# Kernel tuning notes

Measured on AMD Instinct MI355X. Metric: run time of the kernel, lower is better.

## Reference

```python
import jax, jax.numpy as jnp
import numpy as np

# Problem dims
N_LIG, N_PROT = 10000, 40000
N = N_LIG + N_PROT            # total nodes in batched graph
E = 400000                    # total edges (avg degree 8)
B = 512                       # number of pocket graphs in batch
F_LIG, F_PROT = 74, 1280      # ligand / protein node feature dims
H, D = 4, 64                  # GAT heads, per-head dim
HD = H * D                    # hidden size == PROJ_DIM == 256


def setup_inputs() -> dict:
    key = jax.random.key(0)
    ks = jax.random.split(key, 16)
    s = jnp.float32(0.05)  # keep activations tame
    return {
        "ligand_x":  jax.random.normal(ks[0], (N_LIG, F_LIG), jnp.float32),
        "protein_x": jax.random.normal(ks[1], (N_PROT, F_PROT), jnp.float32),
        "W_lig":  jax.random.normal(ks[2], (F_LIG, HD), jnp.float32) * s,
        "W_prot": jax.random.normal(ks[3], (F_PROT, HD), jnp.float32) * s,
        "W1":     jax.random.normal(ks[4], (HD, HD), jnp.float32) * s,
        "a1_src": jax.random.normal(ks[5], (H, D), jnp.float32) * s,
        "a1_dst": jax.random.normal(ks[6], (H, D), jnp.float32) * s,
        "W2":     jax.random.normal(ks[7], (HD, HD), jnp.float32) * s,
        "a2_src": jax.random.normal(ks[8], (H, D), jnp.float32) * s,
        "a2_dst": jax.random.normal(ks[9], (H, D), jnp.float32) * s,
        "W_out":  jax.random.normal(ks[10], (HD + 1, 1), jnp.float32) * s,
        "b_out":  jnp.zeros((1,), jnp.float32),
        "edge_src":  jax.random.randint(ks[11], (E,), 0, N, jnp.int32),
        "edge_dst":  jax.random.randint(ks[12], (E,), 0, N, jnp.int32),
        "graph_ids": jnp.sort(jax.random.randint(ks[13], (N,), 0, B, jnp.int32)),
        "scores":    jax.random.uniform(ks[14], (B, 1), jnp.float32),
    }


def _gat_layer(x, W, a_src, a_dst, src, dst):
    """Multi-head GAT layer over an edge list. x:[N,HD] -> [N,HD]."""
    n = x.shape[0]
    h = (x @ W).reshape(n, H, D)                               # [N,H,D]
    att_s = jnp.einsum('nhd,hd->nh', h, a_src)                 # [N,H]
    att_d = jnp.einsum('nhd,hd->nh', h, a_dst)
    e = jax.nn.leaky_relu(att_s[src] + att_d[dst], 0.2)        # [E,H]
    # edge softmax over incoming edges of each destination node
    m = jax.ops.segment_max(e, dst, num_segments=n)            # [N,H]
    w = jnp.exp(e - m[dst])                                    # [E,H]
    denom = jax.ops.segment_sum(w, dst, num_segments=n)        # [N,H]
    agg = jax.ops.segment_sum(h[src] * w[..., None], dst, num_segments=n)  # [N,H,D]
    out = agg / (denom[..., None] + 1e-9)
    return jax.nn.elu(out).reshape(n, HD)


def reference(ligand_x, protein_x, W_lig, W_prot, W1, a1_src, a1_dst,
              W2, a2_src, a2_dst, W_out, b_out,
              edge_src, edge_dst, graph_ids, scores):
    # per-node-type input projection into shared hidden space
    x = jnp.concatenate([ligand_x @ W_lig, protein_x @ W_prot], axis=0)  # [N,HD]
    h = _gat_layer(x, W1, a1_src, a1_dst, edge_src, edge_dst)
    h = _gat_layer(h, W2, a2_src, a2_dst, edge_src, edge_dst)
    # mean pooling per graph -> [B, PROJ_DIM]
    gsum = jax.ops.segment_sum(h, graph_ids, num_segments=B)
    cnt = jax.ops.segment_sum(jnp.ones((h.shape[0], 1), h.dtype), graph_ids, num_segments=B)
    pooled = gsum / jnp.maximum(cnt, 1.0)
    # concat docking score, final linear (dropout is identity at eval)
    feat = jnp.concatenate([pooled, scores], axis=1)           # [B, PROJ_DIM+1]
    return feat @ W_out + b_out                                 # [B,1]
```

## Files before the change

kernel.cpp:

```cpp
#include <hip/hip_runtime.h>
#include <hip/hip_bf16.h>

#define N_LIG   10000
#define N_PROT  40000
#define NN      50000
#define EDGES   400000
#define BATCH   512
#define F_LIG   74
#define F_PROT  1280
#define HD      256
#define HEADS   4
#define DIM     64

typedef __bf16 bf16x8 __attribute__((ext_vector_type(8)));
typedef __bf16 bf16x4 __attribute__((ext_vector_type(4)));
typedef float  f32x4  __attribute__((ext_vector_type(4)));


__global__ void k_hist(const int* __restrict__ dst, int* __restrict__ counts, int E) {
    int e = blockIdx.x * blockDim.x + threadIdx.x;
    if (e < E) atomicAdd(&counts[dst[e]], 1);
}

__global__ __launch_bounds__(1024) void k_scan1(const int* __restrict__ counts,
                                                int* __restrict__ incl,
                                                int* __restrict__ bsum, int N) {
    __shared__ int tmp[1024];
    int i = blockIdx.x * 1024 + threadIdx.x;
    int v = (i < N) ? counts[i] : 0;
    tmp[threadIdx.x] = v;
    __syncthreads();
    for (int off = 1; off < 1024; off <<= 1) {
        int add = (threadIdx.x >= (unsigned)off) ? tmp[threadIdx.x - off] : 0;
        __syncthreads();
        tmp[threadIdx.x] += add;
        __syncthreads();
    }
    if (i < N) incl[i] = tmp[threadIdx.x];
    if (threadIdx.x == 1023) bsum[blockIdx.x] = tmp[1023];
}

__global__ void k_scan2(int* __restrict__ bsum, int nb, int* __restrict__ row_ptr, int N, int E) {
    if (threadIdx.x == 0 && blockIdx.x == 0) {
        int run = 0;
        for (int i = 0; i < nb; ++i) { int v = bsum[i]; bsum[i] = run; run += v; }
        row_ptr[N] = E;
    }
}

__global__ __launch_bounds__(1024) void k_scan3(const int* __restrict__ incl,
                                                const int* __restrict__ counts,
                                                const int* __restrict__ bsum,
                                                int* __restrict__ row_ptr, int N) {
    int i = blockIdx.x * 1024 + threadIdx.x;
    if (i < N) row_ptr[i] = bsum[blockIdx.x] + incl[i] - counts[i];
}

__global__ void k_scatter(const int* __restrict__ src, const int* __restrict__ dst,
                          const int* __restrict__ row_ptr, int* __restrict__ cursor,
                          int* __restrict__ csr_src, int E) {
    int e = blockIdx.x * blockDim.x + threadIdx.x;
    if (e < E) {
        int d = dst[e];
        int pos = row_ptr[d] + atomicAdd(&cursor[d], 1);
        csr_src[pos] = src[e];
    }
}

__global__ __launch_bounds__(256) void k_wcvt(const float* __restrict__ W,
                                              __bf16* __restrict__ Bt, int K, int Kp) {
    int n = blockIdx.x;
    for (int k = threadIdx.x; k < Kp; k += blockDim.x)
        Bt[(size_t)n * Kp + k] = (k < K) ? (__bf16)W[(size_t)k * HD + n] : (__bf16)0.f;
}

__global__ __launch_bounds__(128) void k_apad(const float* __restrict__ A, float* __restrict__ Ap) {
    int row = blockIdx.x, t = threadIdx.x;
    if (t < 96) Ap[(size_t)row * 96 + t] = (t < F_LIG) ? A[(size_t)row * F_LIG + t] : 0.f;
}

__device__ __forceinline__ void gload16(const void* g, void* l) {
    __builtin_amdgcn_global_load_lds(
        (const __attribute__((address_space(1))) void*)g,
        (__attribute__((address_space(3))) void*)l, 16, 0, 0);
}

template <int MODE>
__global__ __launch_bounds__(256, MODE ? 4 : 5)
void mfma_gemm(const float* __restrict__ A, const __bf16* __restrict__ Bt,
               float* __restrict__ C,
               __bf16* __restrict__ Hbf, float* __restrict__ atts, float* __restrict__ attd,
               const float* __restrict__ a_src, const float* __restrict__ a_dst,
               int M, int K, int Kp) {
    __shared__ __align__(16) unsigned char smem[32768];
    float*  sA = (float*)smem;
    __bf16* sB = (__bf16*)(smem + 16384);

    int tid  = threadIdx.x;
    int bm   = blockIdx.y * 64;
    int bn   = blockIdx.x * 128;
    int lane = tid & 63, wave = tid >> 6;
    int wr   = wave >> 1, wc = wave & 1;
    int l15  = lane & 15, quad = lane >> 4;

    f32x4 acc[2][4];
    #pragma unroll
    for (int i = 0; i < 2; ++i)
        #pragma unroll
        for (int j = 0; j < 4; ++j)
            acc[i][j] = (f32x4){0.f, 0.f, 0.f, 0.f};

    int caA = wave * 2;
    int rlA = lane >> 3, csA = (lane & 7) ^ rlA;
    int rlB = lane >> 2, csB = (lane & 3) ^ (rlB & 3);

    int gmA[2];
    const __bf16* gB[2];
    #pragma unroll
    for (int it = 0; it < 2; ++it) {
        int gm = bm + (caA + it) * 8 + rlA;
        gmA[it] = (gm < M) ? gm : (M - 1);
        gB[it] = Bt + (size_t)(bn + (caA + it) * 16 + rlB) * Kp + csB * 8;
    }

    auto stage = [&](int buf, int k0) {
        #pragma unroll
        for (int it = 0; it < 2; ++it)
            gload16(A + (size_t)gmA[it] * K + k0 + csA * 4,
                    sA + buf * 2048 + (caA + it) * 256);
        #pragma unroll
        for (int it = 0; it < 2; ++it)
            gload16(gB[it] + k0,
                    sB + buf * 4096 + (caA + it) * 512);
    };

    int nsteps = K >> 5;
    stage(0, 0);
    __syncthreads();

    for (int s = 0; s < nsteps; ++s) {
        int cur = s & 1;
        if (s + 1 < nsteps) stage(cur ^ 1, (s + 1) * 32);

        bf16x8 bfr[4];
        #pragma unroll
        for (int j = 0; j < 4; ++j) {
            int rowb = wc * 64 + j * 16 + l15;
            int ch = quad ^ (l15 & 3);
            bfr[j] = *(const bf16x8*)&sB[cur * 4096 + rowb * 32 + ch * 8];
        }
        bf16x8 af[2], al[2];
        #pragma unroll
        for (int i = 0; i < 2; ++i) {
            int rowa = wr * 32 + i * 16 + l15;
            int ch0 = (quad * 2)     ^ (l15 & 7);
            int ch1 = (quad * 2 + 1) ^ (l15 & 7);
            f32x4 p0 = *(const f32x4*)&sA[cur * 2048 + rowa * 32 + ch0 * 4];
            f32x4 p1 = *(const f32x4*)&sA[cur * 2048 + rowa * 32 + ch1 * 4];
            #pragma unroll
            for (int c = 0; c < 8; ++c) {
                float x = (c < 4) ? p0[c] : p1[c - 4];
                __bf16 h = (__bf16)x;
                af[i][c] = h;
                if (MODE) al[i][c] = (__bf16)(x - (float)h);
            }
        }

        #pragma unroll
        for (int i = 0; i < 2; ++i)
            #pragma unroll
            for (int j = 0; j < 4; ++j) {
                acc[i][j] = __builtin_amdgcn_mfma_f32_16x16x32_bf16(af[i], bfr[j], acc[i][j], 0, 0, 0);
                if (MODE)
                    acc[i][j] = __builtin_amdgcn_mfma_f32_16x16x32_bf16(al[i], bfr[j], acc[i][j], 0, 0, 0);
            }

        __syncthreads();
    }

    if (MODE == 0) {
        #pragma unroll
        for (int i = 0; i < 2; ++i)
            #pragma unroll
            for (int r = 0; r < 4; ++r) {
                int m = bm + wr * 32 + i * 16 + quad * 4 + r;
                if (m < M) {
                    #pragma unroll
                    for (int j = 0; j < 4; ++j)
                        C[(size_t)m * HD + bn + wc * 64 + j * 16 + l15] = acc[i][j][r];
                }
            }
    } else {
        int head = (bn >> 6) + wc;
        float as[4], ad2[4];
        #pragma unroll
        for (int j = 0; j < 4; ++j) {
            as[j]  = a_src[head * DIM + j * 16 + l15];
            ad2[j] = a_dst[head * DIM + j * 16 + l15];
        }
        #pragma unroll
        for (int i = 0; i < 2; ++i)
            #pragma unroll
            for (int r = 0; r < 4; ++r) {
                int m = bm + wr * 32 + i * 16 + quad * 4 + r;
                bool ok = m < M;
                float s = 0.f, t = 0.f;
                #pragma unroll
                for (int j = 0; j < 4; ++j) {
                    float v = acc[i][j][r];
                    if (ok) Hbf[(size_t)m * HD + head * DIM + j * 16 + l15] = (__bf16)v;
                    s += v * as[j];
                    t += v * ad2[j];
                }
                #pragma unroll
                for (int mask = 1; mask <= 8; mask <<= 1) {
                    s += __shfl_xor(s, mask, 64);
                    t += __shfl_xor(t, mask, 64);
                }
                if (ok && l15 == 0) {
                    atts[m * HEADS + head] = s;
                    attd[m * HEADS + head] = t;
                }
            }
    }
}

__global__ __launch_bounds__(256) void gat_agg(const __bf16* __restrict__ hW,
                                               const float* __restrict__ att_s,
                                               const float* __restrict__ att_d,
                                               const int* __restrict__ row_ptr,
                                               const int* __restrict__ csr_src,
                                               float* __restrict__ out, int N) {
    int n = blockIdx.x;
    int t = threadIdx.x;
    int lane = t & 63, head = t >> 6;
    int r0 = row_ptr[n], deg = row_ptr[n + 1] - r0;
    float ad = att_d[n * HEADS + head];

    float m = -INFINITY;
    for (int base = 0; base < deg; base += 64) {
        int i = base + lane;
        float e = -INFINITY;
        if (i < deg) {
            int s = csr_src[r0 + i];
            float x = att_s[s * HEADS + head] + ad;
            e = (x >= 0.f) ? x : 0.2f * x;
        }
        for (int off = 32; off > 0; off >>= 1) e = fmaxf(e, __shfl_xor(e, off, 64));
        m = fmaxf(m, e);
    }

    f32x4 acc4 = (f32x4){0.f, 0.f, 0.f, 0.f};
    float wsum = 0.f;
    int sub = lane >> 4;
    int dq  = lane & 15;
    for (int base = 0; base < deg; base += 64) {
        int i = base + lane;
        float w = 0.f; int s = 0;
        if (i < deg) {
            s = csr_src[r0 + i];
            float x = att_s[s * HEADS + head] + ad;
            x = (x >= 0.f) ? x : 0.2f * x;
            w = expf(x - m);
        }
        wsum += w;
        int cnt = min(64, deg - base);
        for (int j0 = 0; j0 < cnt; j0 += 8) {
            #pragma unroll
            for (int g = 0; g < 2; ++g) {
                int e0 = j0 + g * 4 + sub;
                int ec = min(e0, cnt - 1);
                int   sj = __shfl(s, ec, 64);
                float wj = __shfl(w, ec, 64);
                if (e0 >= cnt) wj = 0.f;
                bf16x4 v4 = *(const bf16x4*)&hW[(size_t)sj * HD + head * DIM + dq * 4];
                #pragma unroll
                for (int c = 0; c < 4; ++c) acc4[c] += wj * (float)v4[c];
            }
        }
    }
    #pragma unroll
    for (int c = 0; c < 4; ++c) {
        acc4[c] += __shfl_xor(acc4[c], 16, 64);
        acc4[c] += __shfl_xor(acc4[c], 32, 64);
    }
    for (int off = 32; off > 0; off >>= 1) wsum += __shfl_xor(wsum, off, 64);
    if (sub == 0) {
        float inv = 1.f / (wsum + 1e-9f);
        f32x4 o;
        #pragma unroll
        for (int c = 0; c < 4; ++c) {
            float v = acc4[c] * inv;
            o[c] = (v > 0.f) ? v : expm1f(v);
        }
        *(f32x4*)&out[(size_t)n * HD + head * DIM + dq * 4] = o;
    }
}

__global__ __launch_bounds__(256) void pool_out(const float* __restrict__ h,
                                                const int* __restrict__ gid,
                                                const float* __restrict__ W_out,
                                                const float* __restrict__ b_out,
                                                const float* __restrict__ scores,
                                                float* __restrict__ out, int N) {
    int b = blockIdx.x;
    int j = threadIdx.x;
    int l = 0, r = N;
    while (l < r) { int mid = (l + r) >> 1; if (gid[mid] < b) l = mid + 1; else r = mid; }
    int lo = l;
    r = N;
    while (l < r) { int mid = (l + r) >> 1; if (gid[mid] < b + 1) l = mid + 1; else r = mid; }
    int hi = l;

    float sum = 0.f;
    for (int n = lo; n < hi; ++n) sum += h[(size_t)n * HD + j];
    int cnt = hi - lo;
    float pooled = sum / fmaxf((float)cnt, 1.f);
    float val = pooled * W_out[j];

    __shared__ float red[256];
    red[j] = val;
    __syncthreads();
    for (int s = 128; s > 0; s >>= 1) {
        if (j < s) red[j] += red[j + s];
        __syncthreads();
    }
    if (j == 0) {
        out[b] = red[0] + scores[b] * W_out[HD] + b_out[0];
    }
}


static inline size_t al256(size_t x) { return (x + 255) & ~(size_t)255; }

#define KP_LIG  96
#define KP_PROT 1280
#define KP_HID  256

extern "C" void kernel_launch(void* const* d_in, const int* in_sizes, int n_in,
                              void* d_out, int out_size, void* d_ws, size_t ws_size,
                              hipStream_t stream) {
    const float* ligand_x  = (const float*)d_in[0];
    const float* protein_x = (const float*)d_in[1];
    const float* W_lig     = (const float*)d_in[2];
    const float* W_prot    = (const float*)d_in[3];
    const float* W1        = (const float*)d_in[4];
    const float* a1_src    = (const float*)d_in[5];
    const float* a1_dst    = (const float*)d_in[6];
    const float* W2        = (const float*)d_in[7];
    const float* a2_src    = (const float*)d_in[8];
    const float* a2_dst    = (const float*)d_in[9];
    const float* W_out     = (const float*)d_in[10];
    const float* b_out     = (const float*)d_in[11];
    const int*   edge_src  = (const int*)d_in[12];
    const int*   edge_dst  = (const int*)d_in[13];
    const int*   graph_ids = (const int*)d_in[14];
    const float* scores    = (const float*)d_in[15];
    float* out = (float*)d_out;

    char* w = (char*)d_ws;
    float*  xbuf = (float*)w;           w += al256((size_t)NN * HD * 4);
    __bf16* Hbf  = (__bf16*)w;          w += al256((size_t)NN * HD * 2);
    float* atts = (float*)w;            w += al256((size_t)NN * HEADS * 4);
    float* attd = (float*)w;            w += al256((size_t)NN * HEADS * 4);
    int* counts  = (int*)w;             w += al256((size_t)NN * 4);
    int* incl    = (int*)w;             w += al256((size_t)NN * 4);
    int* bsum    = (int*)w;             w += al256(64 * 4);
    int* row_ptr = (int*)w;             w += al256((size_t)(NN + 1) * 4);
    int* cursor  = (int*)w;             w += al256((size_t)NN * 4);
    int* csr_src = (int*)w;             w += al256((size_t)EDGES * 4);
    __bf16* Bt_lig  = (__bf16*)w;       w += al256((size_t)HD * KP_LIG * 2);
    __bf16* Bt_prot = (__bf16*)w;       w += al256((size_t)HD * KP_PROT * 2);
    __bf16* Bt_W1   = (__bf16*)w;       w += al256((size_t)HD * KP_HID * 2);
    __bf16* Bt_W2   = (__bf16*)w;       w += al256((size_t)HD * KP_HID * 2);
    float* Apad     = (float*)w;        w += al256((size_t)N_LIG * KP_LIG * 4);

    const int NB_SCAN = (NN + 1023) / 1024;

    hipMemsetAsync(counts, 0, (size_t)NN * 4, stream);
    hipMemsetAsync(cursor, 0, (size_t)NN * 4, stream);

    k_wcvt<<<HD, 256, 0, stream>>>(W_lig,  Bt_lig,  F_LIG,  KP_LIG);
    k_wcvt<<<HD, 256, 0, stream>>>(W_prot, Bt_prot, F_PROT, KP_PROT);
    k_wcvt<<<HD, 256, 0, stream>>>(W1,     Bt_W1,   HD,     KP_HID);
    k_wcvt<<<HD, 256, 0, stream>>>(W2,     Bt_W2,   HD,     KP_HID);
    k_apad<<<N_LIG, 128, 0, stream>>>(ligand_x, Apad);

    k_hist<<<(EDGES + 255) / 256, 256, 0, stream>>>(edge_dst, counts, EDGES);
    k_scan1<<<NB_SCAN, 1024, 0, stream>>>(counts, incl, bsum, NN);
    k_scan2<<<1, 1, 0, stream>>>(bsum, NB_SCAN, row_ptr, NN, EDGES);
    k_scan3<<<NB_SCAN, 1024, 0, stream>>>(incl, counts, bsum, row_ptr, NN);
    k_scatter<<<(EDGES + 255) / 256, 256, 0, stream>>>(edge_src, edge_dst, row_ptr,
                                                       cursor, csr_src, EDGES);

    mfma_gemm<0><<<dim3(2, (N_LIG + 63) / 64), 256, 0, stream>>>(
        Apad, Bt_lig, xbuf, nullptr, nullptr, nullptr, nullptr, nullptr,
        N_LIG, KP_LIG, KP_LIG);
    mfma_gemm<0><<<dim3(2, (N_PROT + 63) / 64), 256, 0, stream>>>(
        protein_x, Bt_prot, xbuf + (size_t)N_LIG * HD, nullptr, nullptr, nullptr,
        nullptr, nullptr, N_PROT, KP_PROT, KP_PROT);

    mfma_gemm<1><<<dim3(2, (NN + 63) / 64), 256, 0, stream>>>(
        xbuf, Bt_W1, nullptr, Hbf, atts, attd, a1_src, a1_dst, NN, KP_HID, KP_HID);
    gat_agg<<<NN, 256, 0, stream>>>(Hbf, atts, attd, row_ptr, csr_src, xbuf, NN);

    mfma_gemm<1><<<dim3(2, (NN + 63) / 64), 256, 0, stream>>>(
        xbuf, Bt_W2, nullptr, Hbf, atts, attd, a2_src, a2_dst, NN, KP_HID, KP_HID);
    gat_agg<<<NN, 256, 0, stream>>>(Hbf, atts, attd, row_ptr, csr_src, xbuf, NN);

    pool_out<<<BATCH, 256, 0, stream>>>(xbuf, graph_ids, W_out, b_out, scores, out, NN);
}
```

Measured before the change: 746.8 us.

## Triple-buffer GEMM loads with explicit waitcnt and remap blocks across XCDs

The MFMA GEMM moves from double to triple buffering in shared memory (48KB), prefetching two K-steps ahead. The full __syncthreads is replaced by targeted vmcnt/lgkmcnt waits plus raw barriers, so global loads stay in flight across iterations. The grid is flattened to 1D and block ids are remapped so that consecutive tiles, which share A rows, land on the same XCD for better L2 reuse. The cost is a larger LDS footprint and lower occupancy (launch bounds drop to 3 blocks per CU), and the hand-counted vmcnt values must match the number of issued loads.

```diff
diff --git a/kernel.cpp b/kernel.cpp
--- a/kernel.cpp
+++ b/kernel.cpp
@@ -85,20 +85,27 @@
         (__attribute__((address_space(3))) void*)l, 16, 0, 0);
 }
 
+__device__ __forceinline__ int xcd_swz(int orig, int nwg) {
+    int q = nwg >> 3, r = nwg & 7;
+    int xcd = orig & 7, idx = orig >> 3;
+    return (xcd < r ? xcd * (q + 1) : r * (q + 1) + (xcd - r) * q) + idx;
+}
+
 template <int MODE>
-__global__ __launch_bounds__(256, MODE ? 4 : 5)
+__global__ __launch_bounds__(256, 3)
 void mfma_gemm(const float* __restrict__ A, const __bf16* __restrict__ Bt,
                float* __restrict__ C,
                __bf16* __restrict__ Hbf, float* __restrict__ atts, float* __restrict__ attd,
                const float* __restrict__ a_src, const float* __restrict__ a_dst,
-               int M, int K, int Kp) {
-    __shared__ __align__(16) unsigned char smem[32768];
+               int M, int K, int Kp, int nwg) {
+    __shared__ __align__(16) unsigned char smem[49152];
     float*  sA = (float*)smem;
-    __bf16* sB = (__bf16*)(smem + 16384);
-
+    __bf16* sB = (__bf16*)(smem + 24576);
+
+    int wg   = xcd_swz(blockIdx.x, nwg);
     int tid  = threadIdx.x;
-    int bm   = blockIdx.y * 64;
-    int bn   = blockIdx.x * 128;
+    int bm   = (wg >> 1) * 64;
+    int bn   = (wg & 1) * 128;
     int lane = tid & 63, wave = tid >> 6;
     int wr   = wave >> 1, wc = wave & 1;
     int l15  = lane & 15, quad = lane >> 4;
@@ -135,12 +142,20 @@
     };
 
     int nsteps = K >> 5;
+
     stage(0, 0);
-    __syncthreads();
-
+    if (nsteps > 1) {
+        stage(1, 32);
+        asm volatile("s_waitcnt vmcnt(4)" ::: "memory");
+    } else {
+        asm volatile("s_waitcnt vmcnt(0)" ::: "memory");
+    }
+    __builtin_amdgcn_s_barrier();
+    __builtin_amdgcn_sched_barrier(0);
+
+    int cur = 0, stg = 2;
     for (int s = 0; s < nsteps; ++s) {
-        int cur = s & 1;
-        if (s + 1 < nsteps) stage(cur ^ 1, (s + 1) * 32);
+        if (s + 2 < nsteps) stage(stg, (s + 2) * 32);
 
         bf16x8 bfr[4];
         #pragma unroll
@@ -175,7 +190,15 @@
                     acc[i][j] = __builtin_amdgcn_mfma_f32_16x16x32_bf16(al[i], bfr[j], acc[i][j], 0, 0, 0);
             }
 
-        __syncthreads();
+        asm volatile("s_waitcnt lgkmcnt(0)" ::: "memory");
+        __builtin_amdgcn_sched_barrier(0);
+        if (s + 2 < nsteps)      asm volatile("s_waitcnt vmcnt(4)" ::: "memory");
+        else if (s + 1 < nsteps) asm volatile("s_waitcnt vmcnt(0)" ::: "memory");
+        __builtin_amdgcn_s_barrier();
+        __builtin_amdgcn_sched_barrier(0);
+
+        cur = (cur == 2) ? 0 : cur + 1;
+        stg = (stg == 2) ? 0 : stg + 1;
     }
 
     if (MODE == 0) {
@@ -393,19 +416,31 @@
     k_scatter<<<(EDGES + 255) / 256, 256, 0, stream>>>(edge_src, edge_dst, row_ptr,
                                                        cursor, csr_src, EDGES);
 
-    mfma_gemm<0><<<dim3(2, (N_LIG + 63) / 64), 256, 0, stream>>>(
-        Apad, Bt_lig, xbuf, nullptr, nullptr, nullptr, nullptr, nullptr,
-        N_LIG, KP_LIG, KP_LIG);
-    mfma_gemm<0><<<dim3(2, (N_PROT + 63) / 64), 256, 0, stream>>>(
-        protein_x, Bt_prot, xbuf + (size_t)N_LIG * HD, nullptr, nullptr, nullptr,
-        nullptr, nullptr, N_PROT, KP_PROT, KP_PROT);
-
-    mfma_gemm<1><<<dim3(2, (NN + 63) / 64), 256, 0, stream>>>(
-        xbuf, Bt_W1, nullptr, Hbf, atts, attd, a1_src, a1_dst, NN, KP_HID, KP_HID);
+    {
+        int nwg = 2 * ((N_LIG + 63) / 64);
+        mfma_gemm<0><<<nwg, 256, 0, stream>>>(
+            Apad, Bt_lig, xbuf, nullptr, nullptr, nullptr, nullptr, nullptr,
+            N_LIG, KP_LIG, KP_LIG, nwg);
+    }
+    {
+        int nwg = 2 * ((N_PROT + 63) / 64);
+        mfma_gemm<0><<<nwg, 256, 0, stream>>>(
+            protein_x, Bt_prot, xbuf + (size_t)N_LIG * HD, nullptr, nullptr, nullptr,
+            nullptr, nullptr, N_PROT, KP_PROT, KP_PROT, nwg);
+    }
+
+    {
+        int nwg = 2 * ((NN + 63) / 64);
+        mfma_gemm<1><<<nwg, 256, 0, stream>>>(
+            xbuf, Bt_W1, nullptr, Hbf, atts, attd, a1_src, a1_dst, NN, KP_HID, KP_HID, nwg);
+    }
     gat_agg<<<NN, 256, 0, stream>>>(Hbf, atts, attd, row_ptr, csr_src, xbuf, NN);
 
-    mfma_gemm<1><<<dim3(2, (NN + 63) / 64), 256, 0, stream>>>(
-        xbuf, Bt_W2, nullptr, Hbf, atts, attd, a2_src, a2_dst, NN, KP_HID, KP_HID);
+    {
+        int nwg = 2 * ((NN + 63) / 64);
+        mfma_gemm<1><<<nwg, 256, 0, stream>>>(
+            xbuf, Bt_W2, nullptr, Hbf, atts, attd, a2_src, a2_dst, NN, KP_HID, KP_HID, nwg);
+    }
     gat_agg<<<NN, 256, 0, stream>>>(Hbf, atts, attd, row_ptr, csr_src, xbuf, NN);
 
     pool_out<<<BATCH, 256, 0, stream>>>(xbuf, graph_ids, W_out, b_out, scores, out, NN);
```

After: 726.5 us. 1.03x faster.
